# Kernel tuning notes

Hardware: AMD Instinct MI355X
Metric: run time of the kernel (lower is better)

The kernel has to match this reference:

```python
import jax, jax.numpy as jnp
import numpy as np

ALPHA = 0.001  # heb_lr
EPS = 1e-12    # F.normalize default eps


def setup_inputs() -> dict:
    key = jax.random.key(0)
    k1, k2 = jax.random.split(key)
    x = jax.random.normal(k1, (1, 8192), dtype=jnp.float32)
    # fc.weight ~ Uniform(0, 0.5), shape [out_dim, in_dim]
    W = jax.random.uniform(k2, (4096, 8192), dtype=jnp.float32) * 0.5
    return {"x": x, "W": W}


def reference(x, W):
    # Linear projection (no bias): [1, in] @ [in, out] -> [1, out]
    y = x @ W.T
    # F.normalize(y, p=2, dim=1)
    nrm = jnp.maximum(jnp.linalg.norm(y, axis=1, keepdims=True), EPS)
    y_n = y / nrm

    # Hebbian / Sanger (GHA) weight update, using the INITIAL weight for the
    # decorrelation term (as in the torch code).
    yv = y_n[0]  # [out]
    xv = x[0]    # [in]
    # einsum('jk,lkm,m->jl', W^T, itensors, y) with itensors[l,k,m]=1 iff k==m<=l
    # is exactly a cumulative sum over k of W[k, :] * y[k]  -> [out, in]
    sanger = yv[:, None] * jnp.cumsum(W * yv[:, None], axis=0)
    W_new = W + ALPHA * (jnp.outer(yv, xv) - sanger)
    return y_n, W_new
```

## Files before the change

kernel.cpp:

```cpp
#include <hip/hip_runtime.h>
#include <math.h>

#define ALPHA 0.001f
#define EPS 1e-12f
#define IN_DIM 8192
#define OUT_DIM 4096
#define COL4 (IN_DIM / 4)
#define NSEG 64
#define SEG_ROWS (OUT_DIM / NSEG)

__global__ __launch_bounds__(256) void k_matvec(const float* __restrict__ W,
                                                const float* __restrict__ x,
                                                float* __restrict__ y) {
    const int wave = threadIdx.x >> 6;
    const int lane = threadIdx.x & 63;
    const int row = blockIdx.x * 4 + wave;
    const float4* Wr = (const float4*)(W + (size_t)row * IN_DIM);
    const float4* xv = (const float4*)x;
    float acc = 0.0f;
#pragma unroll 8
    for (int c = 0; c < COL4 / 64; ++c) {
        float4 w = Wr[lane + c * 64];
        float4 xx = xv[lane + c * 64];
        acc += w.x * xx.x + w.y * xx.y + w.z * xx.z + w.w * xx.w;
    }
#pragma unroll
    for (int off = 32; off; off >>= 1) acc += __shfl_xor(acc, off, 64);
    if (lane == 0) y[row] = acc;
}

__global__ __launch_bounds__(256) void k_norm(const float* __restrict__ y,
                                              float* __restrict__ yn_out,
                                              float* __restrict__ yv_ws) {
    __shared__ float red[4];
    float s = 0.0f;
    for (int i = threadIdx.x; i < OUT_DIM; i += 256) {
        float v = y[i];
        s += v * v;
    }
#pragma unroll
    for (int off = 32; off; off >>= 1) s += __shfl_xor(s, off, 64);
    const int wave = threadIdx.x >> 6;
    const int lane = threadIdx.x & 63;
    if (lane == 0) red[wave] = s;
    __syncthreads();
    const float tot = red[0] + red[1] + red[2] + red[3];
    const float inv = 1.0f / fmaxf(sqrtf(tot), EPS);
    for (int i = threadIdx.x; i < OUT_DIM; i += 256) {
        float v = y[i] * inv;
        yn_out[i] = v;
        yv_ws[i] = v;
    }
}

__global__ __launch_bounds__(256) void k_pseg(const float* __restrict__ W,
                                              const float* __restrict__ yv,
                                              float* __restrict__ P) {
    const int seg = blockIdx.y;
    const int col4 = blockIdx.x * 256 + threadIdx.x;
    const float4* Wp = (const float4*)W;
    const int j0 = seg * SEG_ROWS;
    float4 acc = make_float4(0.f, 0.f, 0.f, 0.f);
#pragma unroll 4
    for (int j = 0; j < SEG_ROWS; ++j) {
        const float yj = yv[j0 + j];
        float4 w = Wp[(size_t)(j0 + j) * COL4 + col4];
        acc.x += w.x * yj;
        acc.y += w.y * yj;
        acc.z += w.z * yj;
        acc.w += w.w * yj;
    }
    ((float4*)P)[(size_t)seg * COL4 + col4] = acc;
}

__global__ __launch_bounds__(256) void k_scan(float* __restrict__ P) {
    const int col4 = blockIdx.x * 256 + threadIdx.x;
    float4* Pp = (float4*)P;
    float4 run = make_float4(0.f, 0.f, 0.f, 0.f);
#pragma unroll 4
    for (int s = 0; s < NSEG; ++s) {
        float4 v = Pp[(size_t)s * COL4 + col4];
        Pp[(size_t)s * COL4 + col4] = run;
        run.x += v.x;
        run.y += v.y;
        run.z += v.z;
        run.w += v.w;
    }
}

__global__ __launch_bounds__(256) void k_update(const float* __restrict__ W,
                                                const float* __restrict__ x,
                                                const float* __restrict__ yv,
                                                const float* __restrict__ E,
                                                float* __restrict__ Wout) {
    const int seg = blockIdx.y;
    const int col4 = blockIdx.x * 256 + threadIdx.x;
    const float4* Wp = (const float4*)W;
    float4* Op = (float4*)Wout;
    float4 run = ((const float4*)E)[(size_t)seg * COL4 + col4];
    const float4 x4 = ((const float4*)x)[col4];
    const int j0 = seg * SEG_ROWS;
#pragma unroll 4
    for (int j = 0; j < SEG_ROWS; ++j) {
        const float yj = yv[j0 + j];
        const size_t idx = (size_t)(j0 + j) * COL4 + col4;
        float4 w = Wp[idx];
        run.x += w.x * yj;
        run.y += w.y * yj;
        run.z += w.z * yj;
        run.w += w.w * yj;
        float4 o;
        o.x = w.x + ALPHA * (yj * x4.x - yj * run.x);
        o.y = w.y + ALPHA * (yj * x4.y - yj * run.y);
        o.z = w.z + ALPHA * (yj * x4.z - yj * run.z);
        o.w = w.w + ALPHA * (yj * x4.w - yj * run.w);
        Op[idx] = o;
    }
}

extern "C" void kernel_launch(void* const* d_in, const int* in_sizes, int n_in,
                              void* d_out, int out_size, void* d_ws, size_t ws_size,
                              hipStream_t stream) {
    const float* x = (const float*)d_in[0];
    const float* W = (const float*)d_in[1];
    float* out = (float*)d_out;
    float* yn_out = out;
    float* Wout = out + OUT_DIM;

    float* y = (float*)d_ws;
    float* P = y + OUT_DIM;

    k_matvec<<<dim3(OUT_DIM / 4), dim3(256), 0, stream>>>(W, x, y);
    k_norm<<<dim3(1), dim3(256), 0, stream>>>(y, yn_out, y);
    k_pseg<<<dim3(COL4 / 256, NSEG), dim3(256), 0, stream>>>(W, y, P);
    k_scan<<<dim3(COL4 / 256), dim3(256), 0, stream>>>(P);
    k_update<<<dim3(COL4 / 256, NSEG), dim3(256), 0, stream>>>(W, x, y, P, Wout);
}
```

Before: 288.9 us.

## Fuse Hebbian pipeline into single cooperative kernel with grid syncs

Replaces the five separate kernels (matvec, norm, segment partial sums, scan, update) with one cooperative kernel using grid-wide syncs. Each block owns a 64-row by 2048-column tile, so W is touched by the same block across phases, which may improve cache reuse. Normalization is folded into scalar factors instead of rewriting y. The cost is grid-sync overhead, a low-parallelism scan phase, scalar instead of float4 accesses in the update, and limited occupancy of one 1024-thread block per CU.

```diff
diff --git a/kernel.cpp b/kernel.cpp
--- a/kernel.cpp
+++ b/kernel.cpp
@@ -1,4 +1,5 @@
 #include <hip/hip_runtime.h>
+#include <hip/hip_cooperative_groups.h>
 #include <math.h>
 
 #define ALPHA 0.001f
@@ -7,114 +8,132 @@
 #define OUT_DIM 4096
 #define COL4 (IN_DIM / 4)
 #define NSEG 64
-#define SEG_ROWS (OUT_DIM / NSEG)
+#define SEG_ROWS 64
+#define NCC 4
+#define NBLK 256
+#define THREADS 1024
 
-__global__ __launch_bounds__(256) void k_matvec(const float* __restrict__ W,
-                                                const float* __restrict__ x,
-                                                float* __restrict__ y) {
-    const int wave = threadIdx.x >> 6;
-    const int lane = threadIdx.x & 63;
-    const int row = blockIdx.x * 4 + wave;
-    const float4* Wr = (const float4*)(W + (size_t)row * IN_DIM);
-    const float4* xv = (const float4*)x;
-    float acc = 0.0f;
+namespace cg = cooperative_groups;
+
+#define WS_YPART 0
+#define WS_Y     (OUT_DIM * NCC)
+#define WS_P     (WS_Y + OUT_DIM)
+#define WS_SSQ   (WS_P + NSEG * IN_DIM)
+
+__global__ __launch_bounds__(THREADS) void heb_fused(
+    const float* __restrict__ W, const float* __restrict__ x,
+    float* __restrict__ yn, float* __restrict__ Wout, float* __restrict__ ws) {
+    float* ypart = ws + WS_YPART;
+    float* y     = ws + WS_Y;
+    float* P     = ws + WS_P;
+    float* ssq   = ws + WS_SSQ;
+
+    const int b = blockIdx.x;
+    const int t = threadIdx.x;
+    const int s = b >> 2;
+    const int cc = b & 3;
+    const int wave = t >> 6, lane = t & 63;
+
+    cg::grid_group grid = cg::this_grid();
+
+    if (b == 0 && t == 0) *ssq = 0.f;
+
+    {
+        const float4* x4 = (const float4*)x;
+        for (int rr = 0; rr < 4; ++rr) {
+            const int row = s * SEG_ROWS + wave * 4 + rr;
+            const float4* Wr = (const float4*)W + (size_t)row * COL4;
+            float acc = 0.f;
+#pragma unroll
+            for (int k = 0; k < 8; ++k) {
+                const int idx = cc * 512 + k * 64 + lane;
+                float4 w = Wr[idx], xx = x4[idx];
+                acc += w.x * xx.x + w.y * xx.y + w.z * xx.z + w.w * xx.w;
+            }
+#pragma unroll
+            for (int off = 32; off; off >>= 1) acc += __shfl_xor(acc, off, 64);
+            if (lane == 0) ypart[row * NCC + cc] = acc;
+        }
+    }
+    grid.sync();
+
+    {
+        if (t < 16) {
+            const int r = b * 16 + t;
+            const float v = ypart[r * NCC + 0] + ypart[r * NCC + 1] +
+                            ypart[r * NCC + 2] + ypart[r * NCC + 3];
+            y[r] = v;
+            float q = v * v;
+#pragma unroll
+            for (int off = 8; off; off >>= 1) q += __shfl_xor(q, off, 64);
+            if (t == 0) atomicAdd(ssq, q);
+        }
+    }
+    grid.sync();
+
+    float inv;
+    {
+        inv = 1.f / fmaxf(sqrtf(*ssq), EPS);
+        if (t < 16) {
+            const int r = b * 16 + t;
+            yn[r] = y[r] * inv;
+        }
+        const int col4 = cc * 512 + (t & 511);
+        const int half = t >> 9;
+        const float4* W4 = (const float4*)W;
+        const int j0 = s * SEG_ROWS + half * 32;
+        float4 acc = make_float4(0.f, 0.f, 0.f, 0.f);
+#pragma unroll 4
+        for (int j = 0; j < 32; ++j) {
+            const float yj = y[j0 + j];
+            float4 w = W4[(size_t)(j0 + j) * COL4 + col4];
+            acc.x += w.x * yj; acc.y += w.y * yj;
+            acc.z += w.z * yj; acc.w += w.w * yj;
+        }
+        __shared__ float4 comb[512];
+        if (half == 1) comb[t & 511] = acc;
+        __syncthreads();
+        if (half == 0) {
+            const float4 o = comb[t & 511];
+            acc.x += o.x; acc.y += o.y; acc.z += o.z; acc.w += o.w;
+            ((float4*)P)[(size_t)s * COL4 + col4] = acc;
+        }
+    }
+    grid.sync();
+
+    if (b < 128 && t < 16) {
+        const int col4 = b * 16 + t;
+        float4* P4 = (float4*)P;
+        float4 run = make_float4(0.f, 0.f, 0.f, 0.f);
 #pragma unroll 8
-    for (int c = 0; c < COL4 / 64; ++c) {
-        float4 w = Wr[lane + c * 64];
-        float4 xx = xv[lane + c * 64];
-        acc += w.x * xx.x + w.y * xx.y + w.z * xx.z + w.w * xx.w;
+        for (int ss = 0; ss < NSEG; ++ss) {
+            const float4 v = P4[(size_t)ss * COL4 + col4];
+            P4[(size_t)ss * COL4 + col4] = run;
+            run.x += v.x; run.y += v.y; run.z += v.z; run.w += v.w;
+        }
     }
-#pragma unroll
-    for (int off = 32; off; off >>= 1) acc += __shfl_xor(acc, off, 64);
-    if (lane == 0) y[row] = acc;
-}
+    grid.sync();
 
-__global__ __launch_bounds__(256) void k_norm(const float* __restrict__ y,
-                                              float* __restrict__ yn_out,
-                                              float* __restrict__ yv_ws) {
-    __shared__ float red[4];
-    float s = 0.0f;
-    for (int i = threadIdx.x; i < OUT_DIM; i += 256) {
-        float v = y[i];
-        s += v * v;
-    }
-#pragma unroll
-    for (int off = 32; off; off >>= 1) s += __shfl_xor(s, off, 64);
-    const int wave = threadIdx.x >> 6;
-    const int lane = threadIdx.x & 63;
-    if (lane == 0) red[wave] = s;
-    __syncthreads();
-    const float tot = red[0] + red[1] + red[2] + red[3];
-    const float inv = 1.0f / fmaxf(sqrtf(tot), EPS);
-    for (int i = threadIdx.x; i < OUT_DIM; i += 256) {
-        float v = y[i] * inv;
-        yn_out[i] = v;
-        yv_ws[i] = v;
-    }
-}
-
-__global__ __launch_bounds__(256) void k_pseg(const float* __restrict__ W,
-                                              const float* __restrict__ yv,
-                                              float* __restrict__ P) {
-    const int seg = blockIdx.y;
-    const int col4 = blockIdx.x * 256 + threadIdx.x;
-    const float4* Wp = (const float4*)W;
-    const int j0 = seg * SEG_ROWS;
-    float4 acc = make_float4(0.f, 0.f, 0.f, 0.f);
+    {
+        const int c0 = cc * 2048 + t;
+        const float a_scale = ALPHA * inv;
+        const float b_scale = ALPHA * inv * inv;
+        const int j0 = s * SEG_ROWS;
+        float run0 = P[(size_t)s * IN_DIM + c0];
+        float run1 = P[(size_t)s * IN_DIM + c0 + 1024];
+        const float xc0 = x[c0], xc1 = x[c0 + 1024];
 #pragma unroll 4
-    for (int j = 0; j < SEG_ROWS; ++j) {
-        const float yj = yv[j0 + j];
-        float4 w = Wp[(size_t)(j0 + j) * COL4 + col4];
-        acc.x += w.x * yj;
-        acc.y += w.y * yj;
-        acc.z += w.z * yj;
-        acc.w += w.w * yj;
-    }
-    ((float4*)P)[(size_t)seg * COL4 + col4] = acc;
-}
-
-__global__ __launch_bounds__(256) void k_scan(float* __restrict__ P) {
-    const int col4 = blockIdx.x * 256 + threadIdx.x;
-    float4* Pp = (float4*)P;
-    float4 run = make_float4(0.f, 0.f, 0.f, 0.f);
-#pragma unroll 4
-    for (int s = 0; s < NSEG; ++s) {
-        float4 v = Pp[(size_t)s * COL4 + col4];
-        Pp[(size_t)s * COL4 + col4] = run;
-        run.x += v.x;
-        run.y += v.y;
-        run.z += v.z;
-        run.w += v.w;
-    }
-}
-
-__global__ __launch_bounds__(256) void k_update(const float* __restrict__ W,
-                                                const float* __restrict__ x,
-                                                const float* __restrict__ yv,
-                                                const float* __restrict__ E,
-                                                float* __restrict__ Wout) {
-    const int seg = blockIdx.y;
-    const int col4 = blockIdx.x * 256 + threadIdx.x;
-    const float4* Wp = (const float4*)W;
-    float4* Op = (float4*)Wout;
-    float4 run = ((const float4*)E)[(size_t)seg * COL4 + col4];
-    const float4 x4 = ((const float4*)x)[col4];
-    const int j0 = seg * SEG_ROWS;
-#pragma unroll 4
-    for (int j = 0; j < SEG_ROWS; ++j) {
-        const float yj = yv[j0 + j];
-        const size_t idx = (size_t)(j0 + j) * COL4 + col4;
-        float4 w = Wp[idx];
-        run.x += w.x * yj;
-        run.y += w.y * yj;
-        run.z += w.z * yj;
-        run.w += w.w * yj;
-        float4 o;
-        o.x = w.x + ALPHA * (yj * x4.x - yj * run.x);
-        o.y = w.y + ALPHA * (yj * x4.y - yj * run.y);
-        o.z = w.z + ALPHA * (yj * x4.z - yj * run.z);
-        o.w = w.w + ALPHA * (yj * x4.w - yj * run.w);
-        Op[idx] = o;
+        for (int j = 0; j < SEG_ROWS; ++j) {
+            const float yj = y[j0 + j];
+            const float aj = a_scale * yj;
+            const float bj = b_scale * yj;
+            const size_t i0 = (size_t)(j0 + j) * IN_DIM + c0;
+            const float w0 = W[i0], w1 = W[i0 + 1024];
+            run0 += w0 * yj;
+            run1 += w1 * yj;
+            Wout[i0]        = w0 + aj * xc0 - bj * run0;
+            Wout[i0 + 1024] = w1 + aj * xc1 - bj * run1;
+        }
     }
 }
 
@@ -124,15 +143,11 @@
     const float* x = (const float*)d_in[0];
     const float* W = (const float*)d_in[1];
     float* out = (float*)d_out;
-    float* yn_out = out;
+    float* yn = out;
     float* Wout = out + OUT_DIM;
+    float* ws = (float*)d_ws;
 
-    float* y = (float*)d_ws;
-    float* P = y + OUT_DIM;
-
-    k_matvec<<<dim3(OUT_DIM / 4), dim3(256), 0, stream>>>(W, x, y);
-    k_norm<<<dim3(1), dim3(256), 0, stream>>>(y, yn_out, y);
-    k_pseg<<<dim3(COL4 / 256, NSEG), dim3(256), 0, stream>>>(W, y, P);
-    k_scan<<<dim3(COL4 / 256), dim3(256), 0, stream>>>(P);
-    k_update<<<dim3(COL4 / 256, NSEG), dim3(256), 0, stream>>>(W, x, y, P, Wout);
+    void* args[] = {(void*)&W, (void*)&x, (void*)&yn, (void*)&Wout, (void*)&ws};
+    hipLaunchCooperativeKernel((const void*)heb_fused, dim3(NBLK), dim3(THREADS),
+                               args, 0, stream);
 }
```

Result: slower. 408.6 us (+41.4%).
